# Performance work log

Measured on AMD Instinct MI355X. Metric: run time of the kernel, lower is better.

## Reference

```python
import jax, jax.numpy as jnp
import numpy as np

SCALE = 10.0
THRESH = 1e-3   # nn.Threshold(eps, 0)
NORM_EPS = 1e-12  # F.normalize default eps
LEAKY_SLOPE = 0.01


def _proj(x, W1, W2):
    # x: [B, C, L]; conv1x1 == channel matmul
    h = jnp.einsum('oc,bcl->bol', W1, x)
    h = jnp.where(h >= 0, h, LEAKY_SLOPE * h)
    return jnp.einsum('oc,bcl->bol', W2, h)


def _l2norm(x):
    # normalize over channel dim (dim=1), torch F.normalize semantics
    n = jnp.sqrt(jnp.sum(x * x, axis=1, keepdims=True))
    return x / jnp.maximum(n, NORM_EPS)


def setup_inputs() -> dict:
    key = jax.random.key(0)
    k1, k2, k3, k4 = jax.random.split(key, 4)
    B, C, L, OUT = 4, 64, 4096, 64
    query = jax.random.normal(k1, (B, C, L), dtype=jnp.float32)
    kv = jax.random.normal(k2, (B, C, L), dtype=jnp.float32)
    W1 = jax.random.normal(k3, (2 * C, C), dtype=jnp.float32) * (1.0 / np.sqrt(C))
    W2 = jax.random.normal(k4, (OUT, 2 * C), dtype=jnp.float32) * (1.0 / np.sqrt(2 * C))
    return {"query": query, "key": kv, "W1": W1, "W2": W2}


def reference(query, key, W1, W2):
    # self_attention=True: query_conv is key_conv (shared weights)
    q = _l2norm(_proj(query, W1, W2))   # [B, O, L]
    k = _l2norm(_proj(key, W1, W2))     # [B, O, L]
    scores = jnp.einsum('bcl,bcm->blm', q, k) * SCALE  # [B, L, L]
    w = jax.nn.softmax(scores, axis=-1)
    return jnp.where(w > THRESH, w, 0.0)
```

## Files before the change

### kernel.cpp

```cpp
#include <hip/hip_runtime.h>
#include <math.h>

#define B 4
#define C 64
#define L 4096
#define OUTC 64
#define SCALE 10.0f
#define THRESH 1e-3f

#define EROW 4100
#define SMEM_E_BYTES (16 * EROW * 2)
#define SMEM_WSUM_OFF SMEM_E_BYTES
#define SMEM_RINV_OFF (SMEM_E_BYTES + 512)
#define SMEM_BYTES (SMEM_E_BYTES + 512 + 64)

typedef float v4f __attribute__((ext_vector_type(4)));
typedef short bf16x8 __attribute__((ext_vector_type(8)));
typedef unsigned short us8 __attribute__((ext_vector_type(8)));
typedef unsigned short us4 __attribute__((ext_vector_type(4)));

__device__ __forceinline__ unsigned short f2bf(float x) {
    unsigned int u = __float_as_uint(x);
    u += 0x7fffu + ((u >> 16) & 1u);
    return (unsigned short)(u >> 16);
}
__device__ __forceinline__ float bf2f(unsigned short h) {
    return __uint_as_float(((unsigned int)h) << 16);
}
__device__ __forceinline__ v4f mfma16(bf16x8 a, bf16x8 b, v4f c) {
    return __builtin_amdgcn_mfma_f32_16x16x32_bf16(a, b, c, 0, 0, 0);
}


__global__ void __launch_bounds__(256) proj_kernel(
    const float* __restrict__ q_in, const float* __restrict__ k_in,
    const float* __restrict__ W1, const float* __restrict__ W2,
    unsigned short* __restrict__ Qh, unsigned short* __restrict__ Ql,
    unsigned short* __restrict__ Kh, unsigned short* __restrict__ Kl)
{
    int bid   = blockIdx.x;
    int xcd   = bid & 7;
    int b     = xcd >> 1;
    int which = (bid >> 3) & 1;
    int lt    = ((bid >> 4) << 1) | (xcd & 1);
    int l0    = lt << 6;
    int t     = threadIdx.x;
    int g     = t >> 6;
    int l     = t & 63;

    const float* __restrict__ src =
        (which ? k_in : q_in) + (size_t)b * C * L + l0 + l;
    unsigned short* __restrict__ dh = which ? Kh : Qh;
    unsigned short* __restrict__ dl = which ? Kl : Ql;

    __shared__ float Ht[128][65];
    __shared__ float red[4][64];

    float xr[C];
    #pragma unroll
    for (int c = 0; c < C; ++c)
        xr[c] = src[(size_t)c * L];

    #pragma unroll 1
    for (int oo = 0; oo < 32; oo += 4) {
        #pragma unroll
        for (int u = 0; u < 4; ++u) {
            int o = g * 32 + oo + u;
            float h0 = 0.f, h1 = 0.f, h2 = 0.f, h3 = 0.f;
            #pragma unroll
            for (int c = 0; c < C; c += 4) {
                h0 = fmaf(W1[o * C + c + 0], xr[c + 0], h0);
                h1 = fmaf(W1[o * C + c + 1], xr[c + 1], h1);
                h2 = fmaf(W1[o * C + c + 2], xr[c + 2], h2);
                h3 = fmaf(W1[o * C + c + 3], xr[c + 3], h3);
            }
            float h = (h0 + h1) + (h2 + h3);
            Ht[o][l] = (h >= 0.0f) ? h : 0.01f * h;
        }
    }
    __syncthreads();

    float y[16];
    #pragma unroll
    for (int u = 0; u < 16; ++u) y[u] = 0.f;

    #pragma unroll 1
    for (int hh = 0; hh < 2 * C; hh += 16) {
        float hr[16];
        #pragma unroll
        for (int r = 0; r < 16; ++r)
            hr[r] = Ht[hh + r][l];
        #pragma unroll
        for (int u = 0; u < 16; ++u) {
            int o = g * 16 + u;
            #pragma unroll
            for (int h = 0; h < 16; ++h)
                y[u] = fmaf(W2[o * (2 * C) + hh + h], hr[h], y[u]);
        }
    }

    float ss = 0.f;
    #pragma unroll
    for (int u = 0; u < 16; ++u) ss = fmaf(y[u], y[u], ss);
    red[g][l] = ss;
    __syncthreads();
    float tot = red[0][l] + red[1][l] + red[2][l] + red[3][l];
    float inv = 1.0f / fmaxf(sqrtf(tot), 1e-12f);

    unsigned short hs[16], ls[16];
    #pragma unroll
    for (int u = 0; u < 16; ++u) {
        float val = y[u] * inv;
        hs[u] = f2bf(val);
        ls[u] = f2bf(val - bf2f(hs[u]));
    }
    {
        int col   = l0 + l;
        int tile  = col >> 4;
        int lnn   = col & 15;
        int chunk = g >> 1;
        int quad0 = (g & 1) * 2;
        size_t base0 = (((size_t)b * 256 + tile) * 2 + chunk) * 512
                     + (size_t)(quad0 * 16 + lnn) * 8;
        size_t base1 = base0 + 128;
        *(us8*)(dh + base0) = *(us8*)&hs[0];
        *(us8*)(dh + base1) = *(us8*)&hs[8];
        *(us8*)(dl + base0) = *(us8*)&ls[0];
        *(us8*)(dl + base1) = *(us8*)&ls[8];
    }
}

#define LOADK(SET, TILE) do {                                            \
    size_t _kb = ((ktb + (size_t)(TILE)) * 2) * 512 + (size_t)lane * 8;  \
    SET##h0 = *(const bf16x8*)(Kh + _kb);                                \
    SET##l0 = *(const bf16x8*)(Kl + _kb);                                \
    SET##h1 = *(const bf16x8*)(Kh + _kb + 512);                          \
    SET##l1 = *(const bf16x8*)(Kl + _kb + 512);                          \
} while (0)

__global__ void __launch_bounds__(512) scores_kernel(
    const unsigned short* __restrict__ Qh, const unsigned short* __restrict__ Ql,
    const unsigned short* __restrict__ Kh, const unsigned short* __restrict__ Kl,
    float* __restrict__ out)
{
    extern __shared__ unsigned char smem[];
    unsigned short* __restrict__ e_t  = (unsigned short*)smem;
    float*          __restrict__ wsum = (float*)(smem + SMEM_WSUM_OFF);
    float*          __restrict__ rinv = (float*)(smem + SMEM_RINV_OFF);

    int bid  = blockIdx.x;
    int xcd  = bid & 7;
    int b    = xcd >> 1;
    int r0   = (((bid >> 3) << 1) | (xcd & 1)) << 4;
    int t    = threadIdx.x;
    int wave = t >> 6;
    int lane = t & 63;
    int quad = lane >> 4;
    int ln   = lane & 15;
    int wave16ln = wave * 16 + ln;
    int rowbase  = quad * 4;

    bf16x8 aQ[2][2];
    {
        size_t rowtile = (size_t)b * 256 + (r0 >> 4);
        #pragma unroll
        for (int c0 = 0; c0 < 2; ++c0) {
            size_t base = (rowtile * 2 + c0) * 512 + (size_t)lane * 8;
            aQ[c0][0] = *(const bf16x8*)(Qh + base);
            aQ[c0][1] = *(const bf16x8*)(Ql + base);
        }
    }

    const size_t ktb = (size_t)b * 256;

    v4f ps = (v4f){0.f, 0.f, 0.f, 0.f};
    bf16x8 Ah0, Al0, Ah1, Al1, Bh0, Bl0, Bh1, Bl1;

#define P1TILE(SET, COL0) do {                                           \
    v4f acc = (v4f){0.f, 0.f, 0.f, 0.f};                                 \
    acc = mfma16(aQ[0][0], SET##h0, acc);                                \
    acc = mfma16(aQ[0][1], SET##h0, acc);                                \
    acc = mfma16(aQ[0][0], SET##l0, acc);                                \
    acc = mfma16(aQ[1][0], SET##h1, acc);                                \
    acc = mfma16(aQ[1][1], SET##h1, acc);                                \
    acc = mfma16(aQ[1][0], SET##l1, acc);                                \
    _Pragma("unroll")                                                    \
    for (int r = 0; r < 4; ++r) {                                        \
        float ev = __expf(fmaf(SCALE, acc[r], -SCALE));                  \
        ps[r] += ev;                                                     \
        e_t[(rowbase + r) * EROW + (COL0) + wave16ln] =                  \
            __builtin_bit_cast(unsigned short, (_Float16)ev);            \
    }                                                                    \
} while (0)

    LOADK(A, wave);
    #pragma unroll 1
    for (int i = 0; i < 32; i += 2) {
        LOADK(B, (i + 1) * 8 + wave);
        P1TILE(A, i * 128);
        if (i + 2 < 32)
            LOADK(A, (i + 2) * 8 + wave);
        P1TILE(B, (i + 1) * 128);
    }

    #pragma unroll
    for (int r = 0; r < 4; ++r) {
        float s = ps[r];
        s += __shfl_xor(s, 1);
        s += __shfl_xor(s, 2);
        s += __shfl_xor(s, 4);
        s += __shfl_xor(s, 8);
        if (ln == 0) wsum[(rowbase + r) * 8 + wave] = s;
    }
    __syncthreads();
    if (t < 16) {
        float s = 0.f;
        #pragma unroll
        for (int w = 0; w < 8; ++w) s += wsum[t * 8 + w];
        rinv[t] = 1.0f / s;
    }
    __syncthreads();

    {
        float* __restrict__ outb = out + ((size_t)b * L + r0) * L;
        int row = t >> 5;
        int c0  = (t & 31) * 4;
        float ri = rinv[row];
        const unsigned short* __restrict__ erow = e_t + (size_t)row * EROW;
        float* __restrict__ orow = outb + (size_t)row * L;

        #pragma unroll 4
        for (int it = 0; it < 32; ++it) {
            int col = it * 128 + c0;
            us4 hv = *(const us4*)(erow + col);
            v4f o;
            #pragma unroll
            for (int j = 0; j < 4; ++j) {
                float w = (float)__builtin_bit_cast(_Float16,
                                                    (unsigned short)hv[j]) * ri;
                o[j] = (w > THRESH) ? w : 0.f;
            }
            __builtin_nontemporal_store(o, (v4f*)(orow + col));
        }
    }
}

extern "C" void kernel_launch(void* const* d_in, const int* in_sizes, int n_in,
                              void* d_out, int out_size, void* d_ws, size_t ws_size,
                              hipStream_t stream) {
    const float* query = (const float*)d_in[0];
    const float* key   = (const float*)d_in[1];
    const float* W1    = (const float*)d_in[2];
    const float* W2    = (const float*)d_in[3];
    float* out = (float*)d_out;

    unsigned short* Qh = (unsigned short*)d_ws;
    unsigned short* Ql = Qh + (size_t)B * L * OUTC;
    unsigned short* Kh = Ql + (size_t)B * L * OUTC;
    unsigned short* Kl = Kh + (size_t)B * L * OUTC;

    hipLaunchKernelGGL(proj_kernel, dim3(512), dim3(256), 0, stream,
                       query, key, W1, W2, Qh, Ql, Kh, Kl);
    hipLaunchKernelGGL(scores_kernel, dim3(1024), dim3(512), SMEM_BYTES, stream,
                       Qh, Ql, Kh, Kl, out);
}
```

Baseline: 377.0 us.

## Cache only part of exp scores in LDS and recompute the remaining columns

The LDS buffer of fp16 exponentials shrinks from all 4096 columns to the first 18 tiles (2304 columns). The remaining tiles are recomputed with MFMA after the row sums are known and written straight to global memory, using scalar nontemporal stores. This cuts LDS use per block, which may let more blocks share a CU. The cost is extra K loads and MFMA work for the recomputed columns, and less coalesced scalar stores for that part of the output. It also drops the explicit double-buffered K prefetch in favour of a single register set with unroll 2.

```diff
diff --git a/kernel.cpp b/kernel.cpp
--- a/kernel.cpp
+++ b/kernel.cpp
@@ -8,7 +8,9 @@
 #define SCALE 10.0f
 #define THRESH 1e-3f
 
-#define EROW 4100
+#define NS 18
+#define SCOLS (NS * 128)
+#define EROW 2308
 #define SMEM_E_BYTES (16 * EROW * 2)
 #define SMEM_WSUM_OFF SMEM_E_BYTES
 #define SMEM_RINV_OFF (SMEM_E_BYTES + 512)
@@ -130,12 +132,22 @@
     }
 }
 
-#define LOADK(SET, TILE) do {                                            \
+#define LOADK(TILE) do {                                                 \
     size_t _kb = ((ktb + (size_t)(TILE)) * 2) * 512 + (size_t)lane * 8;  \
-    SET##h0 = *(const bf16x8*)(Kh + _kb);                                \
-    SET##l0 = *(const bf16x8*)(Kl + _kb);                                \
-    SET##h1 = *(const bf16x8*)(Kh + _kb + 512);                          \
-    SET##l1 = *(const bf16x8*)(Kl + _kb + 512);                          \
+    kh0 = *(const bf16x8*)(Kh + _kb);                                    \
+    kl0 = *(const bf16x8*)(Kl + _kb);                                    \
+    kh1 = *(const bf16x8*)(Kh + _kb + 512);                              \
+    kl1 = *(const bf16x8*)(Kl + _kb + 512);                              \
+} while (0)
+
+#define DOMFMA() do {                                                    \
+    acc = (v4f){0.f, 0.f, 0.f, 0.f};                                     \
+    acc = mfma16(aQ[0][0], kh0, acc);                                    \
+    acc = mfma16(aQ[0][1], kh0, acc);                                    \
+    acc = mfma16(aQ[0][0], kl0, acc);                                    \
+    acc = mfma16(aQ[1][0], kh1, acc);                                    \
+    acc = mfma16(aQ[1][1], kh1, acc);                                    \
+    acc = mfma16(aQ[1][0], kl1, acc);                                    \
 } while (0)
 
 __global__ void __launch_bounds__(512) scores_kernel(
@@ -172,35 +184,29 @@
     }
 
     const size_t ktb = (size_t)b * 256;
-
+    bf16x8 kh0, kl0, kh1, kl1;
+    v4f acc;
     v4f ps = (v4f){0.f, 0.f, 0.f, 0.f};
-    bf16x8 Ah0, Al0, Ah1, Al1, Bh0, Bl0, Bh1, Bl1;
-
-#define P1TILE(SET, COL0) do {                                           \
-    v4f acc = (v4f){0.f, 0.f, 0.f, 0.f};                                 \
-    acc = mfma16(aQ[0][0], SET##h0, acc);                                \
-    acc = mfma16(aQ[0][1], SET##h0, acc);                                \
-    acc = mfma16(aQ[0][0], SET##l0, acc);                                \
-    acc = mfma16(aQ[1][0], SET##h1, acc);                                \
-    acc = mfma16(aQ[1][1], SET##h1, acc);                                \
-    acc = mfma16(aQ[1][0], SET##l1, acc);                                \
-    _Pragma("unroll")                                                    \
-    for (int r = 0; r < 4; ++r) {                                        \
-        float ev = __expf(fmaf(SCALE, acc[r], -SCALE));                  \
-        ps[r] += ev;                                                     \
-        e_t[(rowbase + r) * EROW + (COL0) + wave16ln] =                  \
-            __builtin_bit_cast(unsigned short, (_Float16)ev);            \
-    }                                                                    \
-} while (0)
-
-    LOADK(A, wave);
-    #pragma unroll 1
-    for (int i = 0; i < 32; i += 2) {
-        LOADK(B, (i + 1) * 8 + wave);
-        P1TILE(A, i * 128);
-        if (i + 2 < 32)
-            LOADK(A, (i + 2) * 8 + wave);
-        P1TILE(B, (i + 1) * 128);
+
+    #pragma unroll 2
+    for (int i = 0; i < NS; ++i) {
+        LOADK(i * 8 + wave);
+        DOMFMA();
+        #pragma unroll
+        for (int r = 0; r < 4; ++r) {
+            float ev = __expf(fmaf(SCALE, acc[r], -SCALE));
+            ps[r] += ev;
+            e_t[(rowbase + r) * EROW + i * 128 + wave16ln] =
+                __builtin_bit_cast(unsigned short, (_Float16)ev);
+        }
+    }
+    #pragma unroll 2
+    for (int i = NS; i < 32; ++i) {
+        LOADK(i * 8 + wave);
+        DOMFMA();
+        #pragma unroll
+        for (int r = 0; r < 4; ++r)
+            ps[r] += __expf(fmaf(SCALE, acc[r], -SCALE));
     }
 
     #pragma unroll
@@ -221,16 +227,36 @@
     }
     __syncthreads();
 
+    float rv[4];
+    #pragma unroll
+    for (int r = 0; r < 4; ++r)
+        rv[r] = rinv[rowbase + r];
+
+    float* __restrict__ outb = out + ((size_t)b * L + r0) * L;
+
+    #pragma unroll 2
+    for (int i = NS; i < 32; ++i) {
+        LOADK(i * 8 + wave);
+        DOMFMA();
+        int col = i * 128 + wave16ln;
+        #pragma unroll
+        for (int r = 0; r < 4; ++r) {
+            float w = __expf(fmaf(SCALE, acc[r], -SCALE)) * rv[r];
+            w = (w > THRESH) ? w : 0.f;
+            __builtin_nontemporal_store(
+                w, outb + (size_t)(rowbase + r) * L + col);
+        }
+    }
+
     {
-        float* __restrict__ outb = out + ((size_t)b * L + r0) * L;
         int row = t >> 5;
         int c0  = (t & 31) * 4;
         float ri = rinv[row];
         const unsigned short* __restrict__ erow = e_t + (size_t)row * EROW;
         float* __restrict__ orow = outb + (size_t)row * L;
 
-        #pragma unroll 4
-        for (int it = 0; it < 32; ++it) {
+        #pragma unroll 2
+        for (int it = 0; it < NS; ++it) {
             int col = it * 128 + c0;
             us4 hv = *(const us4*)(erow + col);
             v4f o;
```

Measured after the change: 385.1 us. +2.1%, slower.
